# Optimization experiments

Hardware: AMD Instinct MI355X
Metric: run time of the kernel (lower is better)

## Reference

```python
import jax, jax.numpy as jnp
import numpy as np

# dims (match init_kwargs)
I, H, O, R, S = 4, 2048, 2, 2, 2
GB = 2 * R + I          # gaussian_basis_dim default = 2*rank + input_size = 8
B, T = 32, 1024
NOISE_STD, ALPHA = 0.05, 0.2


def setup_inputs() -> dict:
    key = jax.random.key(0)
    ks = jax.random.split(key, 8)
    inp = jax.random.normal(ks[0], (B, T, I), jnp.float32)
    noise = jax.random.normal(ks[1], (B, T, H), jnp.float32)
    gaussian_basis = jax.random.normal(ks[2], (GB, H), jnp.float32)
    # supports: monotone assignment of neurons to populations (default weights=None path)
    sup = np.zeros((S, H), np.float32)
    l = H // S
    for i in range(S):
        sup[i, l * i:l * (i + 1)] = 1.0
    supports = jnp.asarray(sup)
    wi_weights = jax.random.normal(ks[3], (I, S, GB), jnp.float32)
    m_weights = jax.random.normal(ks[4], (R, S, GB), jnp.float32) / jnp.sqrt(jnp.float32(H))
    n_weights = jax.random.normal(ks[5], (R, S, GB), jnp.float32) / jnp.sqrt(jnp.float32(H))
    wo_weights = jax.random.normal(ks[6], (O, S, GB), jnp.float32) / jnp.float32(H)
    wi_biases = jnp.zeros((I, S), jnp.float32)
    m_biases = jnp.zeros((R, S), jnp.float32)
    n_biases = jnp.zeros((R, S), jnp.float32)
    h0_weights = jnp.zeros((S, GB), jnp.float32)
    return {"input": inp, "noise": noise, "gaussian_basis": gaussian_basis,
            "supports": supports, "wi_weights": wi_weights, "m_weights": m_weights,
            "n_weights": n_weights, "wo_weights": wo_weights, "wi_biases": wi_biases,
            "m_biases": m_biases, "n_biases": n_biases, "h0_weights": h0_weights}


def _proxies(gb, sup, wi_w, m_w, n_w, wo_w, wi_b, m_b, n_b, h0_w):
    # wi: (I, H) = sum_s (wi_w @ gb) * supports + wi_b @ supports
    wi = jnp.einsum('isg,gh,sh->ih', wi_w, gb, sup) + wi_b @ sup
    # m, n: (H, R)
    m = jnp.einsum('rsg,gh,sh->hr', m_w, gb, sup) + (m_b @ sup).T
    n = jnp.einsum('rsg,gh,sh->hr', n_w, gb, sup) + (n_b @ sup).T
    # wo: (H, O)
    wo = jnp.einsum('osg,gh,sh->ho', wo_w, gb, sup)
    # h0: (H,)
    h0 = jnp.einsum('sg,gh,sh->h', h0_w, gb, sup)
    return wi, m, n, wo, h0


def reference(input, noise, gaussian_basis, supports, wi_weights, m_weights,
              n_weights, wo_weights, wi_biases, m_biases, n_biases, h0_weights):
    wi, m, n, wo, h0 = _proxies(gaussian_basis, supports, wi_weights, m_weights,
                                n_weights, wo_weights, wi_biases, m_biases,
                                n_biases, h0_weights)
    inv_h = jnp.float32(1.0 / H)
    h_init = jnp.broadcast_to(h0, (B, H))  # h0 broadcasts over batch as in torch

    # precompute input projection for all steps: (B, T, H)
    u_proj = jnp.einsum('bti,ih->bth', input, wi)

    def step(h, xs):
        noise_t, up_t = xs            # (B, H), (B, H)
        r = jnp.tanh(h)               # r from previous h (matches loop semantics)
        rec = (r @ n) @ m.T * inv_h   # (B,R)@(R,H) low-rank recurrence
        h = h + NOISE_STD * noise_t + ALPHA * (-h + rec + up_t)
        out = jnp.tanh(h) @ wo * inv_h  # (B, O)
        return h, (out, h)

    xs = (jnp.swapaxes(noise, 0, 1), jnp.swapaxes(u_proj, 0, 1))  # (T, B, .)
    _, (outs, trajs) = jax.lax.scan(step, h_init, xs)
    output = jnp.swapaxes(outs, 0, 1)        # (B, T, O)
    trajectories = jnp.swapaxes(trajs, 0, 1)  # (B, T, H)
    return output, trajectories
```

## Files before the change

### kernel.cpp

```cpp
#include <hip/hip_runtime.h>

#define B_DIM 32
#define T_DIM 1024
#define I_DIM 4
#define H_DIM 2048
#define O_DIM 2
#define R_DIM 2
#define S_DIM 2
#define G_DIM 8

#define NOISE_STD 0.05f
#define ALPHA 0.2f
#define INV_H (1.0f / (float)H_DIM)

#define NTHREADS 256
#define NWAVES (NTHREADS / 64)
#define EPT 8
#define PF_DEPTH 4

#define WIW 0
#define MW  64
#define NW  96
#define WOW 128
#define WIB 160
#define MB  168
#define NB  172
#define H0W 176
#define WTOT 192

__device__ __forceinline__ float f4get(const float4 v, int e) {
    return e == 0 ? v.x : e == 1 ? v.y : e == 2 ? v.z : v.w;
}

__device__ __forceinline__ float fast_tanh(float x) {
    float e2;
    float t = x * 2.88539008178f;
    asm("v_exp_f32 %0, %1" : "=v"(e2) : "v"(t));
    float r;
    asm("v_rcp_f32 %0, %1" : "=v"(r) : "v"(e2 + 1.0f));
    return fmaf(-2.0f, r, 1.0f);
}

__device__ __forceinline__ void lds_barrier() {
    asm volatile("s_waitcnt lgkmcnt(0)" ::: "memory");
    __builtin_amdgcn_s_barrier();
    asm volatile("" ::: "memory");
}

#define DPP_ADD_F(x, ctrl) \
    x += __int_as_float(__builtin_amdgcn_update_dpp(0, __float_as_int(x), (ctrl), 0xf, 0xf, true))

__device__ __forceinline__ float wave_reduce63(float x) {
    DPP_ADD_F(x, 0x111);
    DPP_ADD_F(x, 0x112);
    DPP_ADD_F(x, 0x114);
    DPP_ADD_F(x, 0x118);
    DPP_ADD_F(x, 0x142);
    DPP_ADD_F(x, 0x143);
    return x;
}

__global__ __launch_bounds__(NTHREADS, 1) void rnn_kernel(
    const float* __restrict__ input,
    const float* __restrict__ noise,
    const float* __restrict__ gb,
    const float* __restrict__ sup,
    const float* __restrict__ wi_w,
    const float* __restrict__ m_w,
    const float* __restrict__ n_w,
    const float* __restrict__ wo_w,
    const float* __restrict__ wi_b,
    const float* __restrict__ m_b,
    const float* __restrict__ n_b,
    const float* __restrict__ h0_w,
    float* __restrict__ out)
{
    const int b    = blockIdx.x;
    const int tid  = threadIdx.x;
    const int wave = tid >> 6;
    const int lane = tid & 63;

    __shared__ float  s_input[T_DIM * I_DIM];
    __shared__ float2 s_out[T_DIM];
    __shared__ float4 s_part[2][NWAVES];
    __shared__ float  s_w[WTOT];

    {
        const float4* inp4 = (const float4*)(input + (size_t)b * (T_DIM * I_DIM));
        float4* sIn4 = (float4*)s_input;
        #pragma unroll
        for (int k = tid; k < T_DIM * I_DIM / 4; k += NTHREADS) sIn4[k] = inp4[k];

        if (tid < 64)       s_w[tid] = wi_w[tid];
        else if (tid < 96)  s_w[tid] = m_w[tid - 64];
        else if (tid < 128) s_w[tid] = n_w[tid - 96];
        else if (tid < 160) s_w[tid] = wo_w[tid - 128];
        else if (tid < 168) s_w[tid] = wi_b[tid - 160];
        else if (tid < 172) s_w[tid] = m_b[tid - 168];
        else if (tid < 176) s_w[tid] = n_b[tid - 172];
        else if (tid < 192) s_w[tid] = h0_w[tid - 176];
    }
    __syncthreads();

    const int h_off0 = 4 * tid;
    const int h_off1 = 1024 + 4 * tid;

    float wiP[EPT][I_DIM], mP[EPT][R_DIM], nP[EPT][R_DIM], woP[EPT][O_DIM];
    float h_reg[EPT], g_reg[EPT];

    #pragma unroll
    for (int c = 0; c < 2; ++c) {
        const int hb = c == 0 ? h_off0 : h_off1;
        float4 gbv[G_DIM];
        #pragma unroll
        for (int g = 0; g < G_DIM; ++g)
            gbv[g] = *(const float4*)(gb + (size_t)g * H_DIM + hb);
        float4 supv[S_DIM];
        #pragma unroll
        for (int s = 0; s < S_DIM; ++s)
            supv[s] = *(const float4*)(sup + (size_t)s * H_DIM + hb);

        #pragma unroll
        for (int j = 0; j < 4; ++j) {
            const int e = c * 4 + j;
            float gcol[G_DIM];
            #pragma unroll
            for (int g = 0; g < G_DIM; ++g) gcol[g] = f4get(gbv[g], j);

            #pragma unroll
            for (int i = 0; i < I_DIM; ++i) wiP[e][i] = 0.0f;
            #pragma unroll
            for (int r = 0; r < R_DIM; ++r) { mP[e][r] = 0.0f; nP[e][r] = 0.0f; }
            #pragma unroll
            for (int o = 0; o < O_DIM; ++o) woP[e][o] = 0.0f;
            float h0v = 0.0f;

            #pragma unroll
            for (int s = 0; s < S_DIM; ++s) {
                float sv = f4get(supv[s], j);
                #pragma unroll
                for (int i = 0; i < I_DIM; ++i) {
                    float d = 0.0f;
                    #pragma unroll
                    for (int g = 0; g < G_DIM; ++g)
                        d = fmaf(s_w[WIW + (i * S_DIM + s) * G_DIM + g], gcol[g], d);
                    wiP[e][i] = fmaf(sv, d + s_w[WIB + i * S_DIM + s], wiP[e][i]);
                }
                #pragma unroll
                for (int r = 0; r < R_DIM; ++r) {
                    float dm = 0.0f, dn = 0.0f;
                    #pragma unroll
                    for (int g = 0; g < G_DIM; ++g) {
                        dm = fmaf(s_w[MW + (r * S_DIM + s) * G_DIM + g], gcol[g], dm);
                        dn = fmaf(s_w[NW + (r * S_DIM + s) * G_DIM + g], gcol[g], dn);
                    }
                    mP[e][r] = fmaf(sv, dm + s_w[MB + r * S_DIM + s], mP[e][r]);
                    nP[e][r] = fmaf(sv, dn + s_w[NB + r * S_DIM + s], nP[e][r]);
                }
                #pragma unroll
                for (int o = 0; o < O_DIM; ++o) {
                    float d = 0.0f;
                    #pragma unroll
                    for (int g = 0; g < G_DIM; ++g)
                        d = fmaf(s_w[WOW + (o * S_DIM + s) * G_DIM + g], gcol[g], d);
                    woP[e][o] = fmaf(sv, d, woP[e][o]);
                }
                {
                    float d = 0.0f;
                    #pragma unroll
                    for (int g = 0; g < G_DIM; ++g)
                        d = fmaf(s_w[H0W + s * G_DIM + g], gcol[g], d);
                    h0v = fmaf(sv, d, h0v);
                }
            }
            h_reg[e] = h0v;
            g_reg[e] = fast_tanh(h0v);
        }
    }

    #pragma unroll
    for (int e = 0; e < EPT; ++e) {
        nP[e][0]  *= INV_H;  nP[e][1]  *= INV_H;
        woP[e][0] *= INV_H;  woP[e][1] *= INV_H;
    }

    const float4* noi4 = (const float4*)(noise + (size_t)b * T_DIM * H_DIM);
    float4* traj4 = (float4*)(out + (size_t)B_DIM * T_DIM * O_DIM + (size_t)b * T_DIM * H_DIM);
    const int f4_0 = tid;
    const int f4_1 = 256 + tid;

    float4 ring[PF_DEPTH][2];
    #pragma unroll
    for (int d = 0; d < PF_DEPTH; ++d) {
        ring[d][0] = noi4[(size_t)d * 512 + f4_0];
        ring[d][1] = noi4[(size_t)d * 512 + f4_1];
    }

    #pragma unroll 4
    for (int t = 0; t < T_DIM; ++t) {
        const int buf = t & 1;
        const int slot = t & (PF_DEPTH - 1);

        float4 nz0 = ring[slot][0];
        float4 nz1 = ring[slot][1];
        {
            int tp = t + PF_DEPTH; if (tp > T_DIM - 1) tp = T_DIM - 1;
            ring[slot][0] = noi4[(size_t)tp * 512 + f4_0];
            ring[slot][1] = noi4[(size_t)tp * 512 + f4_1];
        }
        const float4 uin = *(const float4*)(s_input + t * I_DIM);

        float p0 = 0.f, p1 = 0.f, p2 = 0.f, p3 = 0.f;
        #pragma unroll
        for (int e = 0; e < EPT; ++e) {
            float g = g_reg[e];
            p0 = fmaf(g, nP[e][0], p0);
            p1 = fmaf(g, nP[e][1], p1);
            p2 = fmaf(g, woP[e][0], p2);
            p3 = fmaf(g, woP[e][1], p3);
        }
        p0 = wave_reduce63(p0);
        p1 = wave_reduce63(p1);
        p2 = wave_reduce63(p2);
        p3 = wave_reduce63(p3);
        if (lane == 63) s_part[buf][wave] = make_float4(p0, p1, p2, p3);
        lds_barrier();

        float4 tot = s_part[buf][0];
        #pragma unroll
        for (int w = 1; w < NWAVES; ++w) {
            float4 q = s_part[buf][w];
            tot.x += q.x; tot.y += q.y; tot.z += q.z; tot.w += q.w;
        }
        if (t > 0 && tid == 0)
            s_out[t - 1] = make_float2(tot.z, tot.w);

        const float k0 = tot.x;
        const float k1 = tot.y;

        float4 tr0, tr1;
        #pragma unroll
        for (int e = 0; e < EPT; ++e) {
            float u = uin.x * wiP[e][0];
            u = fmaf(uin.y, wiP[e][1], u);
            u = fmaf(uin.z, wiP[e][2], u);
            u = fmaf(uin.w, wiP[e][3], u);
            float rec = k0 * mP[e][0];
            rec = fmaf(k1, mP[e][1], rec);
            float nzv = e < 4 ? f4get(nz0, e) : f4get(nz1, e - 4);
            float h = h_reg[e];
            h = h + NOISE_STD * nzv + ALPHA * (rec + u - h);
            h_reg[e] = h;
            g_reg[e] = fast_tanh(h);
            float* trp = e < 4 ? (float*)&tr0 : (float*)&tr1;
            trp[e & 3] = h;
        }
        traj4[(size_t)t * 512 + f4_0] = tr0;
        traj4[(size_t)t * 512 + f4_1] = tr1;
    }

    {
        float p2 = 0.f, p3 = 0.f;
        #pragma unroll
        for (int e = 0; e < EPT; ++e) {
            p2 = fmaf(g_reg[e], woP[e][0], p2);
            p3 = fmaf(g_reg[e], woP[e][1], p3);
        }
        p2 = wave_reduce63(p2);
        p3 = wave_reduce63(p3);
        if (lane == 63) s_part[0][wave] = make_float4(p2, p3, 0.f, 0.f);
        __syncthreads();
        if (tid == 0) {
            float a = 0.f, c = 0.f;
            #pragma unroll
            for (int w = 0; w < NWAVES; ++w) { a += s_part[0][w].x; c += s_part[0][w].y; }
            s_out[T_DIM - 1] = make_float2(a, c);
        }
        __syncthreads();
    }

    {
        float4* outg = (float4*)(out + (size_t)b * T_DIM * O_DIM);
        const float4* outl = (const float4*)s_out;
        outg[tid]       = outl[tid];
        outg[tid + 256] = outl[tid + 256];
    }
}

extern "C" void kernel_launch(void* const* d_in, const int* in_sizes, int n_in,
                              void* d_out, int out_size, void* d_ws, size_t ws_size,
                              hipStream_t stream) {
    rnn_kernel<<<B_DIM, NTHREADS, 0, stream>>>(
        (const float*)d_in[0],
        (const float*)d_in[1],
        (const float*)d_in[2],
        (const float*)d_in[3],
        (const float*)d_in[4],
        (const float*)d_in[5],
        (const float*)d_in[6],
        (const float*)d_in[7],
        (const float*)d_in[8],
        (const float*)d_in[9],
        (const float*)d_in[10],
        (const float*)d_in[11],
        (float*)d_out);
}
```

Measured before the change: 898.5 us.

## Use 512 threads with four elements each and fold alpha into weights

Doubles the block size to 512 threads so each thread owns 4 hidden units instead of 8, which gives more memory-level parallelism per block and shortens per-thread serial work in each timestep. It also pre-scales the m and wi proxies by alpha and rewrites the state update as a fused (1-alpha)*h + base form, saving a few flops per element per step. The cost is a cross-wave reduction over 8 waves instead of 4 on every step's barrier, plus more per-step LDS traffic. The final output copy is reduced to a single float4 per thread to match the new thread count.

```diff
diff --git a/kernel.cpp b/kernel.cpp
--- a/kernel.cpp
+++ b/kernel.cpp
@@ -11,11 +11,12 @@
 
 #define NOISE_STD 0.05f
 #define ALPHA 0.2f
+#define ONE_M_ALPHA (1.0f - ALPHA)
 #define INV_H (1.0f / (float)H_DIM)
 
-#define NTHREADS 256
+#define NTHREADS 512
 #define NWAVES (NTHREADS / 64)
-#define EPT 8
+#define EPT 4
 #define PF_DEPTH 4
 
 #define WIW 0
@@ -102,15 +103,12 @@
     }
     __syncthreads();
 
-    const int h_off0 = 4 * tid;
-    const int h_off1 = 1024 + 4 * tid;
+    const int hb = 4 * tid;
 
     float wiP[EPT][I_DIM], mP[EPT][R_DIM], nP[EPT][R_DIM], woP[EPT][O_DIM];
     float h_reg[EPT], g_reg[EPT];
 
-    #pragma unroll
-    for (int c = 0; c < 2; ++c) {
-        const int hb = c == 0 ? h_off0 : h_off1;
+    {
         float4 gbv[G_DIM];
         #pragma unroll
         for (int g = 0; g < G_DIM; ++g)
@@ -121,11 +119,10 @@
             supv[s] = *(const float4*)(sup + (size_t)s * H_DIM + hb);
 
         #pragma unroll
-        for (int j = 0; j < 4; ++j) {
-            const int e = c * 4 + j;
+        for (int e = 0; e < EPT; ++e) {
             float gcol[G_DIM];
             #pragma unroll
-            for (int g = 0; g < G_DIM; ++g) gcol[g] = f4get(gbv[g], j);
+            for (int g = 0; g < G_DIM; ++g) gcol[g] = f4get(gbv[g], e);
 
             #pragma unroll
             for (int i = 0; i < I_DIM; ++i) wiP[e][i] = 0.0f;
@@ -137,7 +134,7 @@
 
             #pragma unroll
             for (int s = 0; s < S_DIM; ++s) {
-                float sv = f4get(supv[s], j);
+                float sv = f4get(supv[s], e);
                 #pragma unroll
                 for (int i = 0; i < I_DIM; ++i) {
                     float d = 0.0f;
@@ -182,31 +179,28 @@
     for (int e = 0; e < EPT; ++e) {
         nP[e][0]  *= INV_H;  nP[e][1]  *= INV_H;
         woP[e][0] *= INV_H;  woP[e][1] *= INV_H;
+        mP[e][0]  *= ALPHA;  mP[e][1]  *= ALPHA;
+        #pragma unroll
+        for (int i = 0; i < I_DIM; ++i) wiP[e][i] *= ALPHA;
     }
 
     const float4* noi4 = (const float4*)(noise + (size_t)b * T_DIM * H_DIM);
     float4* traj4 = (float4*)(out + (size_t)B_DIM * T_DIM * O_DIM + (size_t)b * T_DIM * H_DIM);
-    const int f4_0 = tid;
-    const int f4_1 = 256 + tid;
-
-    float4 ring[PF_DEPTH][2];
+
+    float4 ring[PF_DEPTH];
     #pragma unroll
-    for (int d = 0; d < PF_DEPTH; ++d) {
-        ring[d][0] = noi4[(size_t)d * 512 + f4_0];
-        ring[d][1] = noi4[(size_t)d * 512 + f4_1];
-    }
+    for (int d = 0; d < PF_DEPTH; ++d)
+        ring[d] = noi4[(size_t)d * 512 + tid];
 
     #pragma unroll 4
     for (int t = 0; t < T_DIM; ++t) {
         const int buf = t & 1;
         const int slot = t & (PF_DEPTH - 1);
 
-        float4 nz0 = ring[slot][0];
-        float4 nz1 = ring[slot][1];
+        float4 nz = ring[slot];
         {
             int tp = t + PF_DEPTH; if (tp > T_DIM - 1) tp = T_DIM - 1;
-            ring[slot][0] = noi4[(size_t)tp * 512 + f4_0];
-            ring[slot][1] = noi4[(size_t)tp * 512 + f4_1];
+            ring[slot] = noi4[(size_t)tp * 512 + tid];
         }
         const float4 uin = *(const float4*)(s_input + t * I_DIM);
 
@@ -238,7 +232,7 @@
         const float k0 = tot.x;
         const float k1 = tot.y;
 
-        float4 tr0, tr1;
+        float4 tr;
         #pragma unroll
         for (int e = 0; e < EPT; ++e) {
             float u = uin.x * wiP[e][0];
@@ -247,16 +241,14 @@
             u = fmaf(uin.w, wiP[e][3], u);
             float rec = k0 * mP[e][0];
             rec = fmaf(k1, mP[e][1], rec);
-            float nzv = e < 4 ? f4get(nz0, e) : f4get(nz1, e - 4);
-            float h = h_reg[e];
-            h = h + NOISE_STD * nzv + ALPHA * (rec + u - h);
+            float nzv = f4get(nz, e);
+            float base = fmaf(NOISE_STD, nzv, u + rec);
+            float h = fmaf(ONE_M_ALPHA, h_reg[e], base);
             h_reg[e] = h;
             g_reg[e] = fast_tanh(h);
-            float* trp = e < 4 ? (float*)&tr0 : (float*)&tr1;
-            trp[e & 3] = h;
-        }
-        traj4[(size_t)t * 512 + f4_0] = tr0;
-        traj4[(size_t)t * 512 + f4_1] = tr1;
+            ((float*)&tr)[e] = h;
+        }
+        traj4[(size_t)t * 512 + tid] = tr;
     }
 
     {
@@ -282,8 +274,7 @@
     {
         float4* outg = (float4*)(out + (size_t)b * T_DIM * O_DIM);
         const float4* outl = (const float4*)s_out;
-        outg[tid]       = outl[tid];
-        outg[tid + 256] = outl[tid + 256];
+        outg[tid] = outl[tid];
     }
 }
 
```

After: 928.6 us. 3.3% more time.

## Move output projection to a separate parallel kernel and pack two batches per block

Applied to the files above, without the earlier changes.

Takes the wo readout out of the sequential recurrence and computes it in a second, highly parallel kernel that reads the stored trajectories back and applies tanh and the wo projection. The recurrent kernel now reduces only two values per step instead of four, packs two batch rows into each 512-thread block, and folds ALPHA into the weights to shorten the per-step update. In exchange the trajectory tensor is read again from memory, a second launch is added, and the barrier now spans eight waves across two independent batches.

```diff
diff --git a/kernel.cpp b/kernel.cpp
--- a/kernel.cpp
+++ b/kernel.cpp
@@ -11,22 +11,24 @@
 
 #define NOISE_STD 0.05f
 #define ALPHA 0.2f
+#define ONE_M_ALPHA (1.0f - ALPHA)
 #define INV_H (1.0f / (float)H_DIM)
 
-#define NTHREADS 256
-#define NWAVES (NTHREADS / 64)
+#define NT1 512
+#define GSIZE 256
 #define EPT 8
 #define PF_DEPTH 4
+
+#define NT2 256
 
 #define WIW 0
 #define MW  64
 #define NW  96
-#define WOW 128
-#define WIB 160
-#define MB  168
-#define NB  172
-#define H0W 176
-#define WTOT 192
+#define WIB 128
+#define MB  136
+#define NB  140
+#define H0W 144
+#define WTOT 160
 
 __device__ __forceinline__ float f4get(const float4 v, int e) {
     return e == 0 ? v.x : e == 1 ? v.y : e == 2 ? v.z : v.w;
@@ -60,7 +62,7 @@
     return x;
 }
 
-__global__ __launch_bounds__(NTHREADS, 1) void rnn_kernel(
+__global__ __launch_bounds__(NT1, 1) void rnn_kernel(
     const float* __restrict__ input,
     const float* __restrict__ noise,
     const float* __restrict__ gb,
@@ -68,44 +70,43 @@
     const float* __restrict__ wi_w,
     const float* __restrict__ m_w,
     const float* __restrict__ n_w,
-    const float* __restrict__ wo_w,
     const float* __restrict__ wi_b,
     const float* __restrict__ m_b,
     const float* __restrict__ n_b,
     const float* __restrict__ h0_w,
     float* __restrict__ out)
 {
-    const int b    = blockIdx.x;
-    const int tid  = threadIdx.x;
-    const int wave = tid >> 6;
-    const int lane = tid & 63;
-
-    __shared__ float  s_input[T_DIM * I_DIM];
-    __shared__ float2 s_out[T_DIM];
-    __shared__ float4 s_part[2][NWAVES];
-    __shared__ float  s_w[WTOT];
+    const int tid   = threadIdx.x;
+    const int wave  = tid >> 6;
+    const int lane  = tid & 63;
+    const int grp   = wave >> 2;
+    const int gtid  = tid & (GSIZE - 1);
+    const int b     = blockIdx.x * 2 + grp;
+
+    __shared__ float s_input[2][T_DIM * I_DIM];
+    __shared__ __align__(16) float2 s_part[2][2][4];
+    __shared__ float s_w[WTOT];
 
     {
         const float4* inp4 = (const float4*)(input + (size_t)b * (T_DIM * I_DIM));
-        float4* sIn4 = (float4*)s_input;
-        #pragma unroll
-        for (int k = tid; k < T_DIM * I_DIM / 4; k += NTHREADS) sIn4[k] = inp4[k];
+        float4* sIn4 = (float4*)s_input[grp];
+        #pragma unroll
+        for (int k = gtid; k < T_DIM * I_DIM / 4; k += GSIZE) sIn4[k] = inp4[k];
 
         if (tid < 64)       s_w[tid] = wi_w[tid];
         else if (tid < 96)  s_w[tid] = m_w[tid - 64];
         else if (tid < 128) s_w[tid] = n_w[tid - 96];
-        else if (tid < 160) s_w[tid] = wo_w[tid - 128];
-        else if (tid < 168) s_w[tid] = wi_b[tid - 160];
-        else if (tid < 172) s_w[tid] = m_b[tid - 168];
-        else if (tid < 176) s_w[tid] = n_b[tid - 172];
-        else if (tid < 192) s_w[tid] = h0_w[tid - 176];
+        else if (tid < 136) s_w[tid] = wi_b[tid - 128];
+        else if (tid < 140) s_w[tid] = m_b[tid - 136];
+        else if (tid < 144) s_w[tid] = n_b[tid - 140];
+        else if (tid < 160) s_w[tid] = h0_w[tid - 144];
     }
     __syncthreads();
 
-    const int h_off0 = 4 * tid;
-    const int h_off1 = 1024 + 4 * tid;
-
-    float wiP[EPT][I_DIM], mP[EPT][R_DIM], nP[EPT][R_DIM], woP[EPT][O_DIM];
+    const int h_off0 = 4 * gtid;
+    const int h_off1 = 1024 + 4 * gtid;
+
+    float wiP[EPT][I_DIM], mP[EPT][R_DIM], nP[EPT][R_DIM];
     float h_reg[EPT], g_reg[EPT];
 
     #pragma unroll
@@ -131,8 +132,6 @@
             for (int i = 0; i < I_DIM; ++i) wiP[e][i] = 0.0f;
             #pragma unroll
             for (int r = 0; r < R_DIM; ++r) { mP[e][r] = 0.0f; nP[e][r] = 0.0f; }
-            #pragma unroll
-            for (int o = 0; o < O_DIM; ++o) woP[e][o] = 0.0f;
             float h0v = 0.0f;
 
             #pragma unroll
@@ -157,14 +156,6 @@
                     mP[e][r] = fmaf(sv, dm + s_w[MB + r * S_DIM + s], mP[e][r]);
                     nP[e][r] = fmaf(sv, dn + s_w[NB + r * S_DIM + s], nP[e][r]);
                 }
-                #pragma unroll
-                for (int o = 0; o < O_DIM; ++o) {
-                    float d = 0.0f;
-                    #pragma unroll
-                    for (int g = 0; g < G_DIM; ++g)
-                        d = fmaf(s_w[WOW + (o * S_DIM + s) * G_DIM + g], gcol[g], d);
-                    woP[e][o] = fmaf(sv, d, woP[e][o]);
-                }
                 {
                     float d = 0.0f;
                     #pragma unroll
@@ -180,14 +171,16 @@
 
     #pragma unroll
     for (int e = 0; e < EPT; ++e) {
-        nP[e][0]  *= INV_H;  nP[e][1]  *= INV_H;
-        woP[e][0] *= INV_H;  woP[e][1] *= INV_H;
+        nP[e][0] *= INV_H;  nP[e][1] *= INV_H;
+        mP[e][0] *= ALPHA;  mP[e][1] *= ALPHA;
+        #pragma unroll
+        for (int i = 0; i < I_DIM; ++i) wiP[e][i] *= ALPHA;
     }
 
     const float4* noi4 = (const float4*)(noise + (size_t)b * T_DIM * H_DIM);
     float4* traj4 = (float4*)(out + (size_t)B_DIM * T_DIM * O_DIM + (size_t)b * T_DIM * H_DIM);
-    const int f4_0 = tid;
-    const int f4_1 = 256 + tid;
+    const int f4_0 = gtid;
+    const int f4_1 = 256 + gtid;
 
     float4 ring[PF_DEPTH][2];
     #pragma unroll
@@ -208,35 +201,25 @@
             ring[slot][0] = noi4[(size_t)tp * 512 + f4_0];
             ring[slot][1] = noi4[(size_t)tp * 512 + f4_1];
         }
-        const float4 uin = *(const float4*)(s_input + t * I_DIM);
-
-        float p0 = 0.f, p1 = 0.f, p2 = 0.f, p3 = 0.f;
+        const float4 uin = *(const float4*)(&s_input[grp][t * I_DIM]);
+
+        float p0 = 0.f, p1 = 0.f;
         #pragma unroll
         for (int e = 0; e < EPT; ++e) {
             float g = g_reg[e];
             p0 = fmaf(g, nP[e][0], p0);
             p1 = fmaf(g, nP[e][1], p1);
-            p2 = fmaf(g, woP[e][0], p2);
-            p3 = fmaf(g, woP[e][1], p3);
         }
         p0 = wave_reduce63(p0);
         p1 = wave_reduce63(p1);
-        p2 = wave_reduce63(p2);
-        p3 = wave_reduce63(p3);
-        if (lane == 63) s_part[buf][wave] = make_float4(p0, p1, p2, p3);
+        if (lane == 63) s_part[buf][grp][wave & 3] = make_float2(p0, p1);
         lds_barrier();
 
-        float4 tot = s_part[buf][0];
-        #pragma unroll
-        for (int w = 1; w < NWAVES; ++w) {
-            float4 q = s_part[buf][w];
-            tot.x += q.x; tot.y += q.y; tot.z += q.z; tot.w += q.w;
-        }
-        if (t > 0 && tid == 0)
-            s_out[t - 1] = make_float2(tot.z, tot.w);
-
-        const float k0 = tot.x;
-        const float k1 = tot.y;
+        const float4* sp = (const float4*)&s_part[buf][grp][0];
+        float4 q0 = sp[0];
+        float4 q1 = sp[1];
+        const float k0 = (q0.x + q0.z) + (q1.x + q1.z);
+        const float k1 = (q0.y + q0.w) + (q1.y + q1.w);
 
         float4 tr0, tr1;
         #pragma unroll
@@ -248,8 +231,8 @@
             float rec = k0 * mP[e][0];
             rec = fmaf(k1, mP[e][1], rec);
             float nzv = e < 4 ? f4get(nz0, e) : f4get(nz1, e - 4);
-            float h = h_reg[e];
-            h = h + NOISE_STD * nzv + ALPHA * (rec + u - h);
+            float base = fmaf(NOISE_STD, nzv, u + rec);
+            float h = fmaf(ONE_M_ALPHA, h_reg[e], base);
             h_reg[e] = h;
             g_reg[e] = fast_tanh(h);
             float* trp = e < 4 ? (float*)&tr0 : (float*)&tr1;
@@ -258,39 +241,91 @@
         traj4[(size_t)t * 512 + f4_0] = tr0;
         traj4[(size_t)t * 512 + f4_1] = tr1;
     }
-
-    {
-        float p2 = 0.f, p3 = 0.f;
+}
+
+__global__ __launch_bounds__(NT2, 1) void out_kernel(
+    const float* __restrict__ gb,
+    const float* __restrict__ sup,
+    const float* __restrict__ wo_w,
+    float* __restrict__ out)
+{
+    const int bid  = blockIdx.x;
+    const int b    = bid >> 6;
+    const int t0   = (bid & 63) << 4;
+    const int tid  = threadIdx.x;
+    const int wave = tid >> 6;
+    const int lane = tid & 63;
+
+    __shared__ __align__(16) float2 s_part[2][4];
+
+    const float* traj = out + (size_t)B_DIM * T_DIM * O_DIM + (size_t)b * T_DIM * H_DIM;
+
+    float woP[EPT][O_DIM];
+    #pragma unroll
+    for (int c = 0; c < 2; ++c) {
+        const int hb = c == 0 ? 4 * tid : 1024 + 4 * tid;
+        float4 gbv[G_DIM];
+        #pragma unroll
+        for (int g = 0; g < G_DIM; ++g)
+            gbv[g] = *(const float4*)(gb + (size_t)g * H_DIM + hb);
+        float4 supv[S_DIM];
+        #pragma unroll
+        for (int s = 0; s < S_DIM; ++s)
+            supv[s] = *(const float4*)(sup + (size_t)s * H_DIM + hb);
+
+        #pragma unroll
+        for (int j = 0; j < 4; ++j) {
+            const int e = c * 4 + j;
+            float gcol[G_DIM];
+            #pragma unroll
+            for (int g = 0; g < G_DIM; ++g) gcol[g] = f4get(gbv[g], j);
+            float w0 = 0.f, w1 = 0.f;
+            #pragma unroll
+            for (int s = 0; s < S_DIM; ++s) {
+                float sv = f4get(supv[s], j);
+                float d0 = 0.f, d1 = 0.f;
+                #pragma unroll
+                for (int g = 0; g < G_DIM; ++g) {
+                    d0 = fmaf(wo_w[(0 * S_DIM + s) * G_DIM + g], gcol[g], d0);
+                    d1 = fmaf(wo_w[(1 * S_DIM + s) * G_DIM + g], gcol[g], d1);
+                }
+                w0 = fmaf(sv, d0, w0);
+                w1 = fmaf(sv, d1, w1);
+            }
+            woP[e][0] = w0 * INV_H;
+            woP[e][1] = w1 * INV_H;
+        }
+    }
+
+    for (int tt = 0; tt < 16; ++tt) {
+        const int t = t0 + tt;
+        const float4 a0 = *(const float4*)(traj + (size_t)t * H_DIM + 4 * tid);
+        const float4 a1 = *(const float4*)(traj + (size_t)t * H_DIM + 1024 + 4 * tid);
+        float p0 = 0.f, p1 = 0.f;
         #pragma unroll
         for (int e = 0; e < EPT; ++e) {
-            p2 = fmaf(g_reg[e], woP[e][0], p2);
-            p3 = fmaf(g_reg[e], woP[e][1], p3);
-        }
-        p2 = wave_reduce63(p2);
-        p3 = wave_reduce63(p3);
-        if (lane == 63) s_part[0][wave] = make_float4(p2, p3, 0.f, 0.f);
+            float h = e < 4 ? f4get(a0, e) : f4get(a1, e - 4);
+            float g = fast_tanh(h);
+            p0 = fmaf(g, woP[e][0], p0);
+            p1 = fmaf(g, woP[e][1], p1);
+        }
+        p0 = wave_reduce63(p0);
+        p1 = wave_reduce63(p1);
+        if (lane == 63) s_part[tt & 1][wave] = make_float2(p0, p1);
         __syncthreads();
         if (tid == 0) {
-            float a = 0.f, c = 0.f;
-            #pragma unroll
-            for (int w = 0; w < NWAVES; ++w) { a += s_part[0][w].x; c += s_part[0][w].y; }
-            s_out[T_DIM - 1] = make_float2(a, c);
-        }
-        __syncthreads();
-    }
-
-    {
-        float4* outg = (float4*)(out + (size_t)b * T_DIM * O_DIM);
-        const float4* outl = (const float4*)s_out;
-        outg[tid]       = outl[tid];
-        outg[tid + 256] = outl[tid + 256];
+            float x = 0.f, y = 0.f;
+            #pragma unroll
+            for (int w = 0; w < 4; ++w) { x += s_part[tt & 1][w].x; y += s_part[tt & 1][w].y; }
+            *(float2*)(out + ((size_t)b * T_DIM + t) * O_DIM) = make_float2(x, y);
+        }
     }
 }
 
 extern "C" void kernel_launch(void* const* d_in, const int* in_sizes, int n_in,
                               void* d_out, int out_size, void* d_ws, size_t ws_size,
                               hipStream_t stream) {
-    rnn_kernel<<<B_DIM, NTHREADS, 0, stream>>>(
+    rnn_kernel<<<B_DIM / 2, NT1, 0, stream>>>(
         (const float*)d_in[0],
         (const float*)d_in[1],
         (const float*)d_in[2],
@@ -298,10 +333,14 @@
         (const float*)d_in[4],
         (const float*)d_in[5],
         (const float*)d_in[6],
-        (const float*)d_in[7],
         (const float*)d_in[8],
         (const float*)d_in[9],
         (const float*)d_in[10],
         (const float*)d_in[11],
         (float*)d_out);
-}
+    out_kernel<<<B_DIM * 64, NT2, 0, stream>>>(
+        (const float*)d_in[2],
+        (const float*)d_in[3],
+        (const float*)d_in[7],
+        (float*)d_out);
+}
```

New measurement: 1.098 ms. +22.2%, slower.
